# Optimization experiments

Hardware: AMD Instinct MI355X
Metric: run time of the kernel (lower is better)

## Reference

```python
import jax, jax.numpy as jnp
import numpy as np

NUM_CLASSES = 1000
SCALE = 1.0

def setup_inputs() -> dict:
    key = jax.random.key(0)
    x = jax.random.normal(key, (32768, NUM_CLASSES), dtype=jnp.float32)
    return {"input": x}

def reference(input) -> jnp.ndarray:
    # residual defaults to input in the torch module
    r = input                                   # [B, C]
    n = NUM_CLASSES
    ra = jnp.abs(r)
    mean = jnp.mean(ra, axis=-1, keepdims=True)
    std = jnp.std(ra, axis=-1, keepdims=True, ddof=1)  # torch.std is unbiased
    w = SCALE * jax.nn.sigmoid((ra - mean) / std)       # [B, C]
    # W = I + 1/(n-1) * diag(w) @ (ones - n*I);  (W r)_i = r_i + w_i/(n-1)*(sum(r) - n*r_i)
    s = jnp.sum(r, axis=-1, keepdims=True)              # [B, 1]
    out = r + w / (n - 1) * (s - n * r)
    return out
```

## Files before the change

kernel.cpp:

```cpp
#include <hip/hip_runtime.h>
#include <math.h>

#define NC   1000
#define NVEC 250
#define WPB  4
#define L2E  1.4426950408889634f

typedef float v4f __attribute__((ext_vector_type(4)));

#if __has_builtin(__builtin_amdgcn_exp2f)
#define FAST_EXP2(x) __builtin_amdgcn_exp2f(x)
#else
#define FAST_EXP2(x) exp2f(x)
#endif

#if __has_builtin(__builtin_amdgcn_rcpf)
#define FAST_RCP(x) __builtin_amdgcn_rcpf(x)
#else
#define FAST_RCP(x) (1.0f / (x))
#endif

__global__ __launch_bounds__(256)
void smooth_filter_kernel(const float* __restrict__ in,
                          float* __restrict__ out,
                          int rows) {
    const int lane = threadIdx.x & 63;
    const int row  = blockIdx.x * WPB + (threadIdx.x >> 6);
    if (row >= rows) return;

    const float4* __restrict__ rp = (const float4*)(in  + (size_t)row * NC);
    v4f*          __restrict__ op = (v4f*)         (out + (size_t)row * NC);

    float4 v[4];
    v[3] = make_float4(0.f, 0.f, 0.f, 0.f);
    v[0] = rp[lane];
    v[1] = rp[lane + 64];
    v[2] = rp[lane + 128];
    const bool tail = (lane < (NVEC - 192));
    if (tail) v[3] = rp[lane + 192];

    float s_r = 0.f, s_a = 0.f, s_a2 = 0.f;
    #pragma unroll
    for (int k = 0; k < 4; ++k) {
        const float a0 = fabsf(v[k].x), a1 = fabsf(v[k].y);
        const float a2 = fabsf(v[k].z), a3 = fabsf(v[k].w);
        s_r  += (v[k].x + v[k].y) + (v[k].z + v[k].w);
        s_a  += (a0 + a1) + (a2 + a3);
        s_a2 += (a0 * a0 + a1 * a1) + (a2 * a2 + a3 * a3);
    }

    #pragma unroll
    for (int off = 32; off > 0; off >>= 1) {
        s_r  += __shfl_xor(s_r,  off, 64);
        s_a  += __shfl_xor(s_a,  off, 64);
        s_a2 += __shfl_xor(s_a2, off, 64);
    }

    const float mean    = s_a * (1.0f / NC);
    const float var     = (s_a2 - (float)NC * mean * mean) * (1.0f / (NC - 1));
    const float inv_std = rsqrtf(var);

    const float kx = -inv_std * L2E;
    const float bx =  mean * inv_std * L2E;
    const float c  = 1.0f / (NC - 1);
    const float cS = c * s_r;
    const float cn = c * (float)NC;

    #pragma unroll
    for (int k = 0; k < 4; ++k) {
        if (k == 3 && !tail) break;
        v4f o;
        {
            const float e = FAST_EXP2(fmaf(fabsf(v[k].x), kx, bx));
            o.x = fmaf(FAST_RCP(1.0f + e), fmaf(-cn, v[k].x, cS), v[k].x);
        }
        {
            const float e = FAST_EXP2(fmaf(fabsf(v[k].y), kx, bx));
            o.y = fmaf(FAST_RCP(1.0f + e), fmaf(-cn, v[k].y, cS), v[k].y);
        }
        {
            const float e = FAST_EXP2(fmaf(fabsf(v[k].z), kx, bx));
            o.z = fmaf(FAST_RCP(1.0f + e), fmaf(-cn, v[k].z, cS), v[k].z);
        }
        {
            const float e = FAST_EXP2(fmaf(fabsf(v[k].w), kx, bx));
            o.w = fmaf(FAST_RCP(1.0f + e), fmaf(-cn, v[k].w, cS), v[k].w);
        }
        __builtin_nontemporal_store(o, &op[lane + 64 * k]);
    }
}

extern "C" void kernel_launch(void* const* d_in, const int* in_sizes, int n_in,
                              void* d_out, int out_size, void* d_ws, size_t ws_size,
                              hipStream_t stream) {
    const float* in  = (const float*)d_in[0];
    float*       out = (float*)d_out;
    const int rows   = in_sizes[0] / NC;
    const int blocks = (rows + WPB - 1) / WPB;
    smooth_filter_kernel<<<blocks, 256, 0, stream>>>(in, out, rows);
}
```

Baseline: 227.2 us.

## Use persistent grid-stride waves with register prefetch of the next row

Switches from one row per wave to a fixed grid of 2048 blocks. Each wave loops over rows with a stride and loads the next row into registers before it computes and stores the current one. The aim is to overlap global-load latency with the reduction, exp and store work and to cut block launch overhead. It adds register pressure from holding two rows per lane, and launch_bounds(256,8) may force spills or limit occupancy.

```diff
diff --git a/kernel.cpp b/kernel.cpp
--- a/kernel.cpp
+++ b/kernel.cpp
@@ -4,6 +4,7 @@
 #define NC   1000
 #define NVEC 250
 #define WPB  4
+#define NBLK 2048
 #define L2E  1.4426950408889634f
 
 typedef float v4f __attribute__((ext_vector_type(4)));
@@ -20,73 +21,106 @@
 #define FAST_RCP(x) (1.0f / (x))
 #endif
 
-__global__ __launch_bounds__(256)
+__global__ __launch_bounds__(256, 8)
 void smooth_filter_kernel(const float* __restrict__ in,
                           float* __restrict__ out,
                           int rows) {
-    const int lane = threadIdx.x & 63;
-    const int row  = blockIdx.x * WPB + (threadIdx.x >> 6);
+    const int lane   = threadIdx.x & 63;
+    const int nwaves = gridDim.x * WPB;
+    const bool tail  = (lane < (NVEC - 192));
+
+    int row = blockIdx.x * WPB + (threadIdx.x >> 6);
     if (row >= rows) return;
 
-    const float4* __restrict__ rp = (const float4*)(in  + (size_t)row * NC);
-    v4f*          __restrict__ op = (v4f*)         (out + (size_t)row * NC);
-
-    float4 v[4];
-    v[3] = make_float4(0.f, 0.f, 0.f, 0.f);
-    v[0] = rp[lane];
-    v[1] = rp[lane + 64];
-    v[2] = rp[lane + 128];
-    const bool tail = (lane < (NVEC - 192));
-    if (tail) v[3] = rp[lane + 192];
-
-    float s_r = 0.f, s_a = 0.f, s_a2 = 0.f;
-    #pragma unroll
-    for (int k = 0; k < 4; ++k) {
-        const float a0 = fabsf(v[k].x), a1 = fabsf(v[k].y);
-        const float a2 = fabsf(v[k].z), a3 = fabsf(v[k].w);
-        s_r  += (v[k].x + v[k].y) + (v[k].z + v[k].w);
-        s_a  += (a0 + a1) + (a2 + a3);
-        s_a2 += (a0 * a0 + a1 * a1) + (a2 * a2 + a3 * a3);
+    float4 nv0, nv1, nv2, nv3;
+    nv3 = make_float4(0.f, 0.f, 0.f, 0.f);
+    {
+        const float4* __restrict__ rp = (const float4*)(in + (size_t)row * NC);
+        nv0 = rp[lane];
+        nv1 = rp[lane + 64];
+        nv2 = rp[lane + 128];
+        if (tail) nv3 = rp[lane + 192];
     }
 
-    #pragma unroll
-    for (int off = 32; off > 0; off >>= 1) {
-        s_r  += __shfl_xor(s_r,  off, 64);
-        s_a  += __shfl_xor(s_a,  off, 64);
-        s_a2 += __shfl_xor(s_a2, off, 64);
-    }
+    while (true) {
+        const float4 v0 = nv0, v1 = nv1, v2 = nv2, v3 = nv3;
+        const int srow = row;
+        row += nwaves;
 
-    const float mean    = s_a * (1.0f / NC);
-    const float var     = (s_a2 - (float)NC * mean * mean) * (1.0f / (NC - 1));
-    const float inv_std = rsqrtf(var);
+        if (row < rows) {
+            const float4* __restrict__ np = (const float4*)(in + (size_t)row * NC);
+            nv0 = np[lane];
+            nv1 = np[lane + 64];
+            nv2 = np[lane + 128];
+            if (tail) nv3 = np[lane + 192];
+        }
 
-    const float kx = -inv_std * L2E;
-    const float bx =  mean * inv_std * L2E;
-    const float c  = 1.0f / (NC - 1);
-    const float cS = c * s_r;
-    const float cn = c * (float)NC;
+        float s_r, s_a, s_a2;
+        {
+            const float a00 = fabsf(v0.x), a01 = fabsf(v0.y), a02 = fabsf(v0.z), a03 = fabsf(v0.w);
+            const float a10 = fabsf(v1.x), a11 = fabsf(v1.y), a12 = fabsf(v1.z), a13 = fabsf(v1.w);
+            const float a20 = fabsf(v2.x), a21 = fabsf(v2.y), a22 = fabsf(v2.z), a23 = fabsf(v2.w);
+            const float a30 = fabsf(v3.x), a31 = fabsf(v3.y), a32 = fabsf(v3.z), a33 = fabsf(v3.w);
+            s_r  = ((v0.x + v0.y) + (v0.z + v0.w)) + ((v1.x + v1.y) + (v1.z + v1.w))
+                 + ((v2.x + v2.y) + (v2.z + v2.w)) + ((v3.x + v3.y) + (v3.z + v3.w));
+            s_a  = ((a00 + a01) + (a02 + a03)) + ((a10 + a11) + (a12 + a13))
+                 + ((a20 + a21) + (a22 + a23)) + ((a30 + a31) + (a32 + a33));
+            s_a2 = ((a00*a00 + a01*a01) + (a02*a02 + a03*a03)) + ((a10*a10 + a11*a11) + (a12*a12 + a13*a13))
+                 + ((a20*a20 + a21*a21) + (a22*a22 + a23*a23)) + ((a30*a30 + a31*a31) + (a32*a32 + a33*a33));
+        }
 
-    #pragma unroll
-    for (int k = 0; k < 4; ++k) {
-        if (k == 3 && !tail) break;
-        v4f o;
+        #pragma unroll
+        for (int off = 32; off > 0; off >>= 1) {
+            s_r  += __shfl_xor(s_r,  off, 64);
+            s_a  += __shfl_xor(s_a,  off, 64);
+            s_a2 += __shfl_xor(s_a2, off, 64);
+        }
+
+        const float mean    = s_a * (1.0f / NC);
+        const float var     = (s_a2 - (float)NC * mean * mean) * (1.0f / (NC - 1));
+        const float inv_std = rsqrtf(var);
+
+        const float kx = -inv_std * L2E;
+        const float bx =  mean * inv_std * L2E;
+        const float c  = 1.0f / (NC - 1);
+        const float cS = c * s_r;
+        const float cn = c * (float)NC;
+
+        v4f* __restrict__ op = (v4f*)(out + (size_t)srow * NC);
         {
-            const float e = FAST_EXP2(fmaf(fabsf(v[k].x), kx, bx));
-            o.x = fmaf(FAST_RCP(1.0f + e), fmaf(-cn, v[k].x, cS), v[k].x);
+            v4f o;
+            o.x = fmaf(FAST_RCP(1.0f + FAST_EXP2(fmaf(fabsf(v0.x), kx, bx))), fmaf(-cn, v0.x, cS), v0.x);
+            o.y = fmaf(FAST_RCP(1.0f + FAST_EXP2(fmaf(fabsf(v0.y), kx, bx))), fmaf(-cn, v0.y, cS), v0.y);
+            o.z = fmaf(FAST_RCP(1.0f + FAST_EXP2(fmaf(fabsf(v0.z), kx, bx))), fmaf(-cn, v0.z, cS), v0.z);
+            o.w = fmaf(FAST_RCP(1.0f + FAST_EXP2(fmaf(fabsf(v0.w), kx, bx))), fmaf(-cn, v0.w, cS), v0.w);
+            __builtin_nontemporal_store(o, &op[lane]);
         }
         {
-            const float e = FAST_EXP2(fmaf(fabsf(v[k].y), kx, bx));
-            o.y = fmaf(FAST_RCP(1.0f + e), fmaf(-cn, v[k].y, cS), v[k].y);
+            v4f o;
+            o.x = fmaf(FAST_RCP(1.0f + FAST_EXP2(fmaf(fabsf(v1.x), kx, bx))), fmaf(-cn, v1.x, cS), v1.x);
+            o.y = fmaf(FAST_RCP(1.0f + FAST_EXP2(fmaf(fabsf(v1.y), kx, bx))), fmaf(-cn, v1.y, cS), v1.y);
+            o.z = fmaf(FAST_RCP(1.0f + FAST_EXP2(fmaf(fabsf(v1.z), kx, bx))), fmaf(-cn, v1.z, cS), v1.z);
+            o.w = fmaf(FAST_RCP(1.0f + FAST_EXP2(fmaf(fabsf(v1.w), kx, bx))), fmaf(-cn, v1.w, cS), v1.w);
+            __builtin_nontemporal_store(o, &op[lane + 64]);
         }
         {
-            const float e = FAST_EXP2(fmaf(fabsf(v[k].z), kx, bx));
-            o.z = fmaf(FAST_RCP(1.0f + e), fmaf(-cn, v[k].z, cS), v[k].z);
+            v4f o;
+            o.x = fmaf(FAST_RCP(1.0f + FAST_EXP2(fmaf(fabsf(v2.x), kx, bx))), fmaf(-cn, v2.x, cS), v2.x);
+            o.y = fmaf(FAST_RCP(1.0f + FAST_EXP2(fmaf(fabsf(v2.y), kx, bx))), fmaf(-cn, v2.y, cS), v2.y);
+            o.z = fmaf(FAST_RCP(1.0f + FAST_EXP2(fmaf(fabsf(v2.z), kx, bx))), fmaf(-cn, v2.z, cS), v2.z);
+            o.w = fmaf(FAST_RCP(1.0f + FAST_EXP2(fmaf(fabsf(v2.w), kx, bx))), fmaf(-cn, v2.w, cS), v2.w);
+            __builtin_nontemporal_store(o, &op[lane + 128]);
         }
-        {
-            const float e = FAST_EXP2(fmaf(fabsf(v[k].w), kx, bx));
-            o.w = fmaf(FAST_RCP(1.0f + e), fmaf(-cn, v[k].w, cS), v[k].w);
+        if (tail) {
+            v4f o;
+            o.x = fmaf(FAST_RCP(1.0f + FAST_EXP2(fmaf(fabsf(v3.x), kx, bx))), fmaf(-cn, v3.x, cS), v3.x);
+            o.y = fmaf(FAST_RCP(1.0f + FAST_EXP2(fmaf(fabsf(v3.y), kx, bx))), fmaf(-cn, v3.y, cS), v3.y);
+            o.z = fmaf(FAST_RCP(1.0f + FAST_EXP2(fmaf(fabsf(v3.z), kx, bx))), fmaf(-cn, v3.z, cS), v3.z);
+            o.w = fmaf(FAST_RCP(1.0f + FAST_EXP2(fmaf(fabsf(v3.w), kx, bx))), fmaf(-cn, v3.w, cS), v3.w);
+            __builtin_nontemporal_store(o, &op[lane + 192]);
         }
-        __builtin_nontemporal_store(o, &op[lane + 64 * k]);
+
+        if (row >= rows) break;
     }
 }
 
@@ -96,6 +130,7 @@
     const float* in  = (const float*)d_in[0];
     float*       out = (float*)d_out;
     const int rows   = in_sizes[0] / NC;
-    const int blocks = (rows + WPB - 1) / WPB;
+    const int waves  = NBLK * WPB;
+    const int blocks = (rows < waves) ? (rows + WPB - 1) / WPB : NBLK;
     smooth_filter_kernel<<<blocks, 256, 0, stream>>>(in, out, rows);
 }
```

Measured after the change: 234.7 us. 1.03x slower.

## Process four rows per wavefront with all loads issued up front

Applied to the files above, without the earlier changes.

Each wavefront now handles four rows instead of one. It issues all 16 float4 loads before any reduction, then reduces and writes rows in pairs with interleaved shuffle reductions. The aim is more memory-level parallelism per wave and fewer blocks, so load latency is hidden better. In exchange, register pressure is much higher, which may cut occupancy. It also gives fewer total waves, 2048 blocks, to spread across the CUs.

```diff
diff --git a/kernel.cpp b/kernel.cpp
--- a/kernel.cpp
+++ b/kernel.cpp
@@ -4,6 +4,7 @@
 #define NC   1000
 #define NVEC 250
 #define WPB  4
+#define RPW  4
 #define L2E  1.4426950408889634f
 
 typedef float v4f __attribute__((ext_vector_type(4)));
@@ -20,73 +21,147 @@
 #define FAST_RCP(x) (1.0f / (x))
 #endif
 
-__global__ __launch_bounds__(256)
+struct Row { float4 c0, c1, c2, c3; };
+
+__device__ __forceinline__ Row load_row(const float* __restrict__ in, int row,
+                                        int lane, bool tail) {
+    const float4* __restrict__ rp = (const float4*)(in + (size_t)row * NC);
+    Row r;
+    r.c0 = rp[lane];
+    r.c1 = rp[lane + 64];
+    r.c2 = rp[lane + 128];
+    r.c3 = tail ? rp[lane + 192] : make_float4(0.f, 0.f, 0.f, 0.f);
+    return r;
+}
+
+__device__ __forceinline__ void accum_chunk(const float4& c, float& sr, float& sa, float& sa2) {
+    const float a0 = fabsf(c.x), a1 = fabsf(c.y), a2 = fabsf(c.z), a3 = fabsf(c.w);
+    sr  += (c.x + c.y) + (c.z + c.w);
+    sa  += (a0 + a1) + (a2 + a3);
+    sa2 += (a0 * a0 + a1 * a1) + (a2 * a2 + a3 * a3);
+}
+
+__device__ __forceinline__ float elem(float x, float kx, float bx, float cn, float cS) {
+    return fmaf(FAST_RCP(1.0f + FAST_EXP2(fmaf(fabsf(x), kx, bx))), fmaf(-cn, x, cS), x);
+}
+
+__device__ __forceinline__ void do_epilogue(const Row& r, float S, float SA, float SA2,
+                                            float* __restrict__ out, int row,
+                                            int lane, bool tail) {
+    const float mean    = SA * (1.0f / NC);
+    const float var     = (SA2 - (float)NC * mean * mean) * (1.0f / (NC - 1));
+    const float inv_std = rsqrtf(var);
+    const float kx = -inv_std * L2E;
+    const float bx =  mean * inv_std * L2E;
+    const float c  = 1.0f / (NC - 1);
+    const float cS = c * S;
+    const float cn = c * (float)NC;
+
+    v4f* __restrict__ op = (v4f*)(out + (size_t)row * NC);
+    {
+        v4f o;
+        o.x = elem(r.c0.x, kx, bx, cn, cS);
+        o.y = elem(r.c0.y, kx, bx, cn, cS);
+        o.z = elem(r.c0.z, kx, bx, cn, cS);
+        o.w = elem(r.c0.w, kx, bx, cn, cS);
+        __builtin_nontemporal_store(o, &op[lane]);
+    }
+    {
+        v4f o;
+        o.x = elem(r.c1.x, kx, bx, cn, cS);
+        o.y = elem(r.c1.y, kx, bx, cn, cS);
+        o.z = elem(r.c1.z, kx, bx, cn, cS);
+        o.w = elem(r.c1.w, kx, bx, cn, cS);
+        __builtin_nontemporal_store(o, &op[lane + 64]);
+    }
+    {
+        v4f o;
+        o.x = elem(r.c2.x, kx, bx, cn, cS);
+        o.y = elem(r.c2.y, kx, bx, cn, cS);
+        o.z = elem(r.c2.z, kx, bx, cn, cS);
+        o.w = elem(r.c2.w, kx, bx, cn, cS);
+        __builtin_nontemporal_store(o, &op[lane + 128]);
+    }
+    if (tail) {
+        v4f o;
+        o.x = elem(r.c3.x, kx, bx, cn, cS);
+        o.y = elem(r.c3.y, kx, bx, cn, cS);
+        o.z = elem(r.c3.z, kx, bx, cn, cS);
+        o.w = elem(r.c3.w, kx, bx, cn, cS);
+        __builtin_nontemporal_store(o, &op[lane + 192]);
+    }
+}
+
+__global__ __launch_bounds__(256, 4)
 void smooth_filter_kernel(const float* __restrict__ in,
                           float* __restrict__ out,
                           int rows) {
-    const int lane = threadIdx.x & 63;
-    const int row  = blockIdx.x * WPB + (threadIdx.x >> 6);
-    if (row >= rows) return;
+    const int  lane = threadIdx.x & 63;
+    const bool tail = (lane < (NVEC - 192));
+    const int  wid  = blockIdx.x * WPB + (threadIdx.x >> 6);
+    const int  row0 = wid * RPW;
+    if (row0 >= rows) return;
 
-    const float4* __restrict__ rp = (const float4*)(in  + (size_t)row * NC);
-    v4f*          __restrict__ op = (v4f*)         (out + (size_t)row * NC);
+    const bool h1 = (row0 + 1) < rows;
+    const bool h2 = (row0 + 2) < rows;
+    const bool h3 = (row0 + 3) < rows;
 
-    float4 v[4];
-    v[3] = make_float4(0.f, 0.f, 0.f, 0.f);
-    v[0] = rp[lane];
-    v[1] = rp[lane + 64];
-    v[2] = rp[lane + 128];
-    const bool tail = (lane < (NVEC - 192));
-    if (tail) v[3] = rp[lane + 192];
+    Row A0 = load_row(in, row0, lane, tail);
+    Row A1, B0, B1;
+    if (h1) A1 = load_row(in, row0 + 1, lane, tail); else A1 = A0;
+    if (h2) B0 = load_row(in, row0 + 2, lane, tail); else B0 = A0;
+    if (h3) B1 = load_row(in, row0 + 3, lane, tail); else B1 = A0;
 
-    float s_r = 0.f, s_a = 0.f, s_a2 = 0.f;
-    #pragma unroll
-    for (int k = 0; k < 4; ++k) {
-        const float a0 = fabsf(v[k].x), a1 = fabsf(v[k].y);
-        const float a2 = fabsf(v[k].z), a3 = fabsf(v[k].w);
-        s_r  += (v[k].x + v[k].y) + (v[k].z + v[k].w);
-        s_a  += (a0 + a1) + (a2 + a3);
-        s_a2 += (a0 * a0 + a1 * a1) + (a2 * a2 + a3 * a3);
+    {
+        float xr = 0.f, xa = 0.f, xa2 = 0.f;
+        float yr = 0.f, ya = 0.f, ya2 = 0.f;
+        accum_chunk(A0.c0, xr, xa, xa2);
+        accum_chunk(A0.c1, xr, xa, xa2);
+        accum_chunk(A0.c2, xr, xa, xa2);
+        accum_chunk(A0.c3, xr, xa, xa2);
+        accum_chunk(A1.c0, yr, ya, ya2);
+        accum_chunk(A1.c1, yr, ya, ya2);
+        accum_chunk(A1.c2, yr, ya, ya2);
+        accum_chunk(A1.c3, yr, ya, ya2);
+
+        #pragma unroll
+        for (int off = 32; off > 0; off >>= 1) {
+            xr  += __shfl_xor(xr,  off, 64);
+            yr  += __shfl_xor(yr,  off, 64);
+            xa  += __shfl_xor(xa,  off, 64);
+            ya  += __shfl_xor(ya,  off, 64);
+            xa2 += __shfl_xor(xa2, off, 64);
+            ya2 += __shfl_xor(ya2, off, 64);
+        }
+
+        do_epilogue(A0, xr, xa, xa2, out, row0, lane, tail);
+        if (h1) do_epilogue(A1, yr, ya, ya2, out, row0 + 1, lane, tail);
     }
 
-    #pragma unroll
-    for (int off = 32; off > 0; off >>= 1) {
-        s_r  += __shfl_xor(s_r,  off, 64);
-        s_a  += __shfl_xor(s_a,  off, 64);
-        s_a2 += __shfl_xor(s_a2, off, 64);
-    }
+    {
+        float xr = 0.f, xa = 0.f, xa2 = 0.f;
+        float yr = 0.f, ya = 0.f, ya2 = 0.f;
+        accum_chunk(B0.c0, xr, xa, xa2);
+        accum_chunk(B0.c1, xr, xa, xa2);
+        accum_chunk(B0.c2, xr, xa, xa2);
+        accum_chunk(B0.c3, xr, xa, xa2);
+        accum_chunk(B1.c0, yr, ya, ya2);
+        accum_chunk(B1.c1, yr, ya, ya2);
+        accum_chunk(B1.c2, yr, ya, ya2);
+        accum_chunk(B1.c3, yr, ya, ya2);
 
-    const float mean    = s_a * (1.0f / NC);
-    const float var     = (s_a2 - (float)NC * mean * mean) * (1.0f / (NC - 1));
-    const float inv_std = rsqrtf(var);
+        #pragma unroll
+        for (int off = 32; off > 0; off >>= 1) {
+            xr  += __shfl_xor(xr,  off, 64);
+            yr  += __shfl_xor(yr,  off, 64);
+            xa  += __shfl_xor(xa,  off, 64);
+            ya  += __shfl_xor(ya,  off, 64);
+            xa2 += __shfl_xor(xa2, off, 64);
+            ya2 += __shfl_xor(ya2, off, 64);
+        }
 
-    const float kx = -inv_std * L2E;
-    const float bx =  mean * inv_std * L2E;
-    const float c  = 1.0f / (NC - 1);
-    const float cS = c * s_r;
-    const float cn = c * (float)NC;
-
-    #pragma unroll
-    for (int k = 0; k < 4; ++k) {
-        if (k == 3 && !tail) break;
-        v4f o;
-        {
-            const float e = FAST_EXP2(fmaf(fabsf(v[k].x), kx, bx));
-            o.x = fmaf(FAST_RCP(1.0f + e), fmaf(-cn, v[k].x, cS), v[k].x);
-        }
-        {
-            const float e = FAST_EXP2(fmaf(fabsf(v[k].y), kx, bx));
-            o.y = fmaf(FAST_RCP(1.0f + e), fmaf(-cn, v[k].y, cS), v[k].y);
-        }
-        {
-            const float e = FAST_EXP2(fmaf(fabsf(v[k].z), kx, bx));
-            o.z = fmaf(FAST_RCP(1.0f + e), fmaf(-cn, v[k].z, cS), v[k].z);
-        }
-        {
-            const float e = FAST_EXP2(fmaf(fabsf(v[k].w), kx, bx));
-            o.w = fmaf(FAST_RCP(1.0f + e), fmaf(-cn, v[k].w, cS), v[k].w);
-        }
-        __builtin_nontemporal_store(o, &op[lane + 64 * k]);
+        if (h2) do_epilogue(B0, xr, xa, xa2, out, row0 + 2, lane, tail);
+        if (h3) do_epilogue(B1, yr, ya, ya2, out, row0 + 3, lane, tail);
     }
 }
 
@@ -96,6 +171,7 @@
     const float* in  = (const float*)d_in[0];
     float*       out = (float*)d_out;
     const int rows   = in_sizes[0] / NC;
-    const int blocks = (rows + WPB - 1) / WPB;
+    const int rpb    = WPB * RPW;
+    const int blocks = (rows + rpb - 1) / rpb;
     smooth_filter_kernel<<<blocks, 256, 0, stream>>>(in, out, rows);
 }
```

Measured after the change: 229.5 us. No clear change (+1.0%).
